# Performance work log

Hardware: AMD Instinct MI355X
Metric: run time of the kernel (lower is better)

The kernel has to match this reference:

```python
import jax, jax.numpy as jnp
import numpy as np

L, H, P = 8192, 512, 512


def setup_inputs() -> dict:
    key = jax.random.key(0)
    ks = jax.random.split(key, 7)
    u = jax.random.normal(ks[0], (L, H), dtype=jnp.float32)
    # diagonal continuous-time state matrix Lambda = Lambda_re + i*Lambda_im (stable: Re < 0)
    Lambda_re = -0.5 * jax.random.uniform(ks[1], (P,), dtype=jnp.float32) - 0.1
    Lambda_im = jnp.pi * jax.random.normal(ks[2], (P,), dtype=jnp.float32)
    # B_tilde (P,H) and C_tilde (H,P) parameterized as real/imag pairs (..., 2)
    B = jax.random.normal(ks[3], (P, H, 2), dtype=jnp.float32) / np.sqrt(2.0 * H)
    C = jax.random.normal(ks[4], (H, P, 2), dtype=jnp.float32) / np.sqrt(2.0 * P)
    D = jax.random.normal(ks[5], (H,), dtype=jnp.float32)
    log_step = jax.random.uniform(ks[6], (P,), dtype=jnp.float32,
                                  minval=np.log(1e-3), maxval=np.log(1e-1))
    return {"u": u, "Lambda_re": Lambda_re, "Lambda_im": Lambda_im,
            "B": B, "C": C, "D": D, "log_step": log_step}


def _binop(qi, qj):
    # binary operator for parallel scan of diagonal linear recurrence
    A_i, Bu_i = qi
    A_j, Bu_j = qj
    return (A_j * A_i, A_j * Bu_i + Bu_j)


def reference(u, Lambda_re, Lambda_im, B, C, D, log_step):
    Lambda = (Lambda_re + 1j * Lambda_im).astype(jnp.complex64)          # (P,)
    B_tilde = (B[..., 0] + 1j * B[..., 1]).astype(jnp.complex64)         # (P,H)
    C_tilde = (C[..., 0] + 1j * C[..., 1]).astype(jnp.complex64)         # (H,P)
    Delta = jnp.exp(log_step)                                            # (P,)
    # zero-order-hold discretization
    Lambda_bar = jnp.exp(Lambda * Delta)                                 # (P,)
    B_bar = ((Lambda_bar - 1.0) / Lambda)[:, None] * B_tilde             # (P,H)
    # Bu_t = B_bar @ u_t for all t  -> (L,P)
    Bu = jnp.einsum('lh,ph->lp', u.astype(jnp.complex64), B_bar)
    A_elems = jnp.broadcast_to(Lambda_bar, (u.shape[0], P))              # (L,P)
    _, xs = jax.lax.associative_scan(_binop, (A_elems, Bu), axis=0)      # (L,P) states
    # y_t = Re(C_tilde @ x_t) + D * u_t
    y = jnp.einsum('lp,hp->lh', xs, C_tilde).real + D * u
    return y
```

## Files before the change

kernel.cpp:

```cpp
#include <hip/hip_runtime.h>
#include <hip/hip_bf16.h>

#define L_DIM 8192
#define H_DIM 512
#define P_DIM 512
#define CHUNK 32
#define NCHUNK (L_DIM / CHUNK)

typedef __attribute__((ext_vector_type(8))) short bf16x8;
typedef __attribute__((ext_vector_type(4))) float f32x4;

__device__ inline short f2bf(float x) {
    union { float f; unsigned u; } v; v.f = x;
    unsigned r = v.u + 0x7fffu + ((v.u >> 16) & 1u);
    return (short)(r >> 16);
}
__device__ inline float bflo2f(unsigned w) {
    union { unsigned u; float f; } v; v.u = w << 16; return v.f;
}
__device__ inline float bfhi2f(unsigned w) {
    union { unsigned u; float f; } v; v.u = w & 0xffff0000u; return v.f;
}

__device__ inline void gload_lds16(const void* g, void* l) {
    __builtin_amdgcn_global_load_lds(
        (const __attribute__((address_space(1))) unsigned int*)g,
        (__attribute__((address_space(3))) unsigned int*)l, 16, 0, 0);
}

__global__ __launch_bounds__(256) void k_prep(
        const float* __restrict__ Lre, const float* __restrict__ Lim,
        const float* __restrict__ Bin, const float* __restrict__ log_step,
        const float* __restrict__ Cin, const float* __restrict__ u,
        short* __restrict__ Bcat, short* __restrict__ Ccat,
        short* __restrict__ u_bf,
        float* __restrict__ lambda_bar, float* __restrict__ lambda_powN) {
    const int blk = blockIdx.x;
    const int tid = threadIdx.x;
    if (blk < P_DIM) {
        int p = blk;
        float lr = Lre[p], li = Lim[p];
        float dt = expf(log_step[p]);
        float ar = lr * dt, ai = li * dt;
        float er = expf(ar);
        float lbr = er * cosf(ai);
        float lbi = er * sinf(ai);
        float nr = lbr - 1.0f, ni = lbi;
        float den = lr * lr + li * li;
        float fr = (nr * lr + ni * li) / den;
        float fi = (ni * lr - nr * li) / den;
        if (tid == 0) {
            lambda_bar[2 * p] = lbr;
            lambda_bar[2 * p + 1] = lbi;
            float eN = expf(ar * (float)CHUNK);
            lambda_powN[2 * p] = eN * cosf(ai * (float)CHUNK);
            lambda_powN[2 * p + 1] = eN * sinf(ai * (float)CHUNK);
        }
        for (int h = tid; h < H_DIM; h += 256) {
            float br = Bin[((size_t)p * H_DIM + h) * 2 + 0];
            float bi = Bin[((size_t)p * H_DIM + h) * 2 + 1];
            Bcat[(size_t)(2 * p) * H_DIM + h] = f2bf(fr * br - fi * bi);
            Bcat[(size_t)(2 * p + 1) * H_DIM + h] = f2bf(fr * bi + fi * br);
        }
    } else if (blk < P_DIM + 1024) {
        int idx = (blk - P_DIM) * 256 + tid;
        int h = idx >> 9, p = idx & 511;
        float cr = Cin[(size_t)idx * 2 + 0];
        float ci = Cin[(size_t)idx * 2 + 1];
        Ccat[(size_t)h * (2 * P_DIM) + 2 * p + 0] = f2bf(cr);
        Ccat[(size_t)h * (2 * P_DIM) + 2 * p + 1] = f2bf(-ci);
    } else {
        int i = (blk - P_DIM - 1024) * 256 + tid;
        const float4* uf = (const float4*)u;
        float4 a0 = uf[(size_t)i * 2];
        float4 a1 = uf[(size_t)i * 2 + 1];
        bf16x8 sv;
        sv[0] = f2bf(a0.x); sv[1] = f2bf(a0.y); sv[2] = f2bf(a0.z); sv[3] = f2bf(a0.w);
        sv[4] = f2bf(a1.x); sv[5] = f2bf(a1.y); sv[6] = f2bf(a1.z); sv[7] = f2bf(a1.w);
        *(bf16x8*)&u_bf[(size_t)i * 8] = sv;
    }
}

template<bool OBF16, bool EPI>
__global__ __launch_bounds__(256) void k_gemm(
        const short* __restrict__ A, const short* __restrict__ B,
        void* __restrict__ Cout, int M, int N, int K, int nwgn,
        const float* __restrict__ Dv, const short* __restrict__ Ubf) {
    __shared__ short As[2][128 * 32];
    __shared__ short Bs[2][128 * 32];
    const int tid = threadIdx.x;
    const int lane = tid & 63;
    const int wid = tid >> 6;
    const int wr = wid >> 1, wc = wid & 1;

    const int nwg = gridDim.x;
    const int orig = blockIdx.x;
    const int id = (orig & 7) * (nwg >> 3) + (orig >> 3);
    const int bm = (id / nwgn) * 128;
    const int bn = (id % nwgn) * 128;

    const int sbyte = wid * 2048 + lane * 16;
    const int srow = sbyte >> 6;
    const int scol = sbyte & 63;

    f32x4 acc[4][4] = {};
    const int arow = wr * 64 + (lane & 15);
    const int brow = wc * 64 + (lane & 15);
    const int kgrp = (lane >> 4) * 8;

    auto stage = [&](int buf, int kk) {
        const char* a0 = (const char*)A + ((size_t)(bm + srow) * K + kk) * 2 + scol;
        gload_lds16(a0, (char*)&As[buf][0] + sbyte);
        const char* a1 = (const char*)A + ((size_t)(bm + srow + 16) * K + kk) * 2 + scol;
        gload_lds16(a1, (char*)&As[buf][0] + sbyte + 1024);
        const char* b0 = (const char*)B + ((size_t)(bn + srow) * K + kk) * 2 + scol;
        gload_lds16(b0, (char*)&Bs[buf][0] + sbyte);
        const char* b1 = (const char*)B + ((size_t)(bn + srow + 16) * K + kk) * 2 + scol;
        gload_lds16(b1, (char*)&Bs[buf][0] + sbyte + 1024);
    };

    stage(0, 0);
    __syncthreads();

    int cur = 0;
    const int nt = K >> 5;
    for (int t = 0; t < nt; ++t) {
        if (t + 1 < nt) stage(cur ^ 1, (t + 1) * 32);
        bf16x8 af[4], bfr[4];
#pragma unroll
        for (int m = 0; m < 4; ++m) af[m] = *(const bf16x8*)&As[cur][(arow + m * 16) * 32 + kgrp];
#pragma unroll
        for (int n = 0; n < 4; ++n) bfr[n] = *(const bf16x8*)&Bs[cur][(brow + n * 16) * 32 + kgrp];
#pragma unroll
        for (int m = 0; m < 4; ++m)
#pragma unroll
            for (int n = 0; n < 4; ++n)
                acc[m][n] = __builtin_amdgcn_mfma_f32_16x16x32_bf16(af[m], bfr[n], acc[m][n], 0, 0, 0);
        __syncthreads();
        cur ^= 1;
    }

    const int fq = lane >> 4, fr = lane & 15;
#pragma unroll
    for (int m = 0; m < 4; ++m) {
#pragma unroll
        for (int n = 0; n < 4; ++n) {
            int col = bn + wc * 64 + n * 16 + fr;
            int row0 = bm + wr * 64 + m * 16 + fq * 4;
#pragma unroll
            for (int j = 0; j < 4; ++j) {
                int row = row0 + j;
                float v = acc[m][n][j];
                if (OBF16) {
                    ((short*)Cout)[(size_t)row * N + col] = f2bf(v);
                } else {
                    if (EPI) {
                        union { unsigned u; float f; } ub;
                        ub.u = ((unsigned)(unsigned short)Ubf[(size_t)row * N + col]) << 16;
                        v += Dv[col] * ub.f;
                    }
                    ((float*)Cout)[(size_t)row * N + col] = v;
                }
            }
        }
    }
}

__global__ __launch_bounds__(256) void k_scan_summary(const unsigned* __restrict__ Bu,
                                                      const float* __restrict__ lambda_bar,
                                                      float* __restrict__ S) {
    int gid = blockIdx.x * blockDim.x + threadIdx.x;
    int c = gid >> 9, p = gid & 511;
    float lr = lambda_bar[2 * p], li = lambda_bar[2 * p + 1];
    float xr = 0.f, xi = 0.f;
    const unsigned* bu = Bu + (size_t)c * CHUNK * P_DIM + p;
#pragma unroll 4
    for (int j = 0; j < CHUNK; ++j) {
        unsigned w = bu[(size_t)j * P_DIM];
        float br = bflo2f(w), bi = bfhi2f(w);
        float nxr = lr * xr - li * xi + br;
        float nxi = lr * xi + li * xr + bi;
        xr = nxr; xi = nxi;
    }
    ((float2*)S)[(size_t)c * P_DIM + p] = make_float2(xr, xi);
}

__global__ __launch_bounds__(512) void k_scan_apply(const unsigned* __restrict__ Bu,
                                                    unsigned* __restrict__ XsB,
                                                    const float* __restrict__ lambda_bar,
                                                    const float* __restrict__ lambda_powN,
                                                    const float* __restrict__ S) {
    const int c = blockIdx.x;
    const int p = threadIdx.x;
    const float lNr = lambda_powN[2 * p], lNi = lambda_powN[2 * p + 1];
    float xr = 0.f, xi = 0.f;
    const float2* Sp = (const float2*)S;
    int d = 0;
    while (d + 8 <= c) {
        float2 sb[8];
#pragma unroll
        for (int j = 0; j < 8; ++j) sb[j] = Sp[(size_t)(d + j) * P_DIM + p];
#pragma unroll
        for (int j = 0; j < 8; ++j) {
            float nxr = lNr * xr - lNi * xi + sb[j].x;
            float nxi = lNr * xi + lNi * xr + sb[j].y;
            xr = nxr; xi = nxi;
        }
        d += 8;
    }
    for (; d < c; ++d) {
        float2 s = Sp[(size_t)d * P_DIM + p];
        float nxr = lNr * xr - lNi * xi + s.x;
        float nxi = lNr * xi + lNi * xr + s.y;
        xr = nxr; xi = nxi;
    }
    const float lr = lambda_bar[2 * p], li = lambda_bar[2 * p + 1];
    const unsigned* bu = Bu + (size_t)c * CHUNK * P_DIM + p;
#pragma unroll 4
    for (int j = 0; j < CHUNK; ++j) {
        unsigned w = bu[(size_t)j * P_DIM];
        float br = bflo2f(w), bi = bfhi2f(w);
        float nxr = lr * xr - li * xi + br;
        float nxi = lr * xi + li * xr + bi;
        xr = nxr; xi = nxi;
        unsigned pk = (unsigned)(unsigned short)f2bf(xr)
                    | ((unsigned)(unsigned short)f2bf(xi) << 16);
        XsB[((size_t)c * CHUNK + j) * P_DIM + p] = pk;
    }
}

extern "C" void kernel_launch(void* const* d_in, const int* in_sizes, int n_in,
                              void* d_out, int out_size, void* d_ws, size_t ws_size,
                              hipStream_t stream) {
    const float* u        = (const float*)d_in[0];
    const float* Lre      = (const float*)d_in[1];
    const float* Lim      = (const float*)d_in[2];
    const float* Bin      = (const float*)d_in[3];
    const float* Cin      = (const float*)d_in[4];
    const float* Dv       = (const float*)d_in[5];
    const float* log_step = (const float*)d_in[6];
    float* y = (float*)d_out;

    char* w = (char*)d_ws;
    size_t off = 0;
    short* Bcat = (short*)(w + off); off += (size_t)2 * P_DIM * H_DIM * 2;
    short* Ccat = (short*)(w + off); off += (size_t)2 * P_DIM * H_DIM * 2;
    float* lamb = (float*)(w + off); off += 2 * P_DIM * 4;
    float* lamN = (float*)(w + off); off += 2 * P_DIM * 4;
    float* S    = (float*)(w + off); off += (size_t)NCHUNK * 2 * P_DIM * 4;
    unsigned* Bu  = (unsigned*)(w + off); off += (size_t)L_DIM * P_DIM * 4;
    unsigned* XsB = (unsigned*)(w + off); off += (size_t)L_DIM * P_DIM * 4;
    short* u_bf   = (short*)(w + off);   off += (size_t)L_DIM * H_DIM * 2;

    k_prep<<<P_DIM + 1024 + 2048, 256, 0, stream>>>(
        Lre, Lim, Bin, log_step, Cin, u, Bcat, Ccat, u_bf, lamb, lamN);
    k_gemm<true, false><<<(L_DIM / 128) * ((2 * P_DIM) / 128), 256, 0, stream>>>(
        u_bf, Bcat, (void*)Bu, L_DIM, 2 * P_DIM, H_DIM, (2 * P_DIM) / 128,
        nullptr, nullptr);
    k_scan_summary<<<(NCHUNK * P_DIM) / 256, 256, 0, stream>>>(Bu, lamb, S);
    k_scan_apply<<<NCHUNK, 512, 0, stream>>>(Bu, XsB, lamb, lamN, S);
    k_gemm<false, true><<<(L_DIM / 128) * (H_DIM / 128), 256, 0, stream>>>(
        (const short*)XsB, Ccat, (void*)y, L_DIM, H_DIM, 2 * P_DIM, H_DIM / 128,
        Dv, u_bf);
}
```

Measured before the change: 81.61 us.

## Triple-buffer GEMM LDS staging with XOR swizzle and narrower tiles for second GEMM

Rewrites the bf16 MFMA GEMM main loop to use three LDS buffers with two tiles in flight, replacing __syncthreads with explicit vmcnt waits and raw barriers. LDS reads and writes get an XOR swizzle to cut bank conflicts on the fragment loads. The output GEMM switches to 128x64 tiles, doubling its workgroup count to fill more CUs. The cost is extra LDS use and hand-written wait counts that must match the number of loads issued per stage.

```diff
diff --git a/kernel.cpp b/kernel.cpp
--- a/kernel.cpp
+++ b/kernel.cpp
@@ -26,6 +26,14 @@
     __builtin_amdgcn_global_load_lds(
         (const __attribute__((address_space(1))) unsigned int*)g,
         (__attribute__((address_space(3))) unsigned int*)l, 16, 0, 0);
+}
+
+template<int N> __device__ inline void waitcnt_vm() {
+    if constexpr (N == 0)      asm volatile("s_waitcnt vmcnt(0)" ::: "memory");
+    else if constexpr (N == 3) asm volatile("s_waitcnt vmcnt(3)" ::: "memory");
+    else if constexpr (N == 4) asm volatile("s_waitcnt vmcnt(4)" ::: "memory");
+    else if constexpr (N == 6) asm volatile("s_waitcnt vmcnt(6)" ::: "memory");
+    else if constexpr (N == 8) asm volatile("s_waitcnt vmcnt(8)" ::: "memory");
 }
 
 __global__ __launch_bounds__(256) void k_prep(
@@ -81,13 +89,16 @@
     }
 }
 
-template<bool OBF16, bool EPI>
+template<int BN, bool OBF16, bool EPI>
 __global__ __launch_bounds__(256) void k_gemm(
         const short* __restrict__ A, const short* __restrict__ B,
         void* __restrict__ Cout, int M, int N, int K, int nwgn,
         const float* __restrict__ Dv, const short* __restrict__ Ubf) {
-    __shared__ short As[2][128 * 32];
-    __shared__ short Bs[2][128 * 32];
+    constexpr int NF = BN / 32;
+    constexpr int LPS = 2 + BN / 64;
+    __shared__ short As[3][128 * 32];
+    __shared__ short Bs[3][BN * 32];
+
     const int tid = threadIdx.x;
     const int lane = tid & 63;
     const int wid = tid >> 6;
@@ -97,55 +108,75 @@
     const int orig = blockIdx.x;
     const int id = (orig & 7) * (nwg >> 3) + (orig >> 3);
     const int bm = (id / nwgn) * 128;
-    const int bn = (id % nwgn) * 128;
-
-    const int sbyte = wid * 2048 + lane * 16;
-    const int srow = sbyte >> 6;
-    const int scol = sbyte & 63;
-
-    f32x4 acc[4][4] = {};
+    const int bn = (id % nwgn) * BN;
+
+    f32x4 acc[4][NF] = {};
     const int arow = wr * 64 + (lane & 15);
-    const int brow = wc * 64 + (lane & 15);
-    const int kgrp = (lane >> 4) * 8;
+    const int brow = wc * (BN / 2) + (lane & 15);
+    const int rslot = (((lane >> 4) ^ (lane & 3) ^ ((lane >> 2) & 3)) << 4);
 
     auto stage = [&](int buf, int kk) {
-        const char* a0 = (const char*)A + ((size_t)(bm + srow) * K + kk) * 2 + scol;
-        gload_lds16(a0, (char*)&As[buf][0] + sbyte);
-        const char* a1 = (const char*)A + ((size_t)(bm + srow + 16) * K + kk) * 2 + scol;
-        gload_lds16(a1, (char*)&As[buf][0] + sbyte + 1024);
-        const char* b0 = (const char*)B + ((size_t)(bn + srow) * K + kk) * 2 + scol;
-        gload_lds16(b0, (char*)&Bs[buf][0] + sbyte);
-        const char* b1 = (const char*)B + ((size_t)(bn + srow + 16) * K + kk) * 2 + scol;
-        gload_lds16(b1, (char*)&Bs[buf][0] + sbyte + 1024);
+#pragma unroll
+        for (int q = 0; q < 2; ++q) {
+            int sb = q * 4096 + tid * 16;
+            int row = sb >> 6, slot = (sb >> 4) & 3;
+            int gs = slot ^ ((row ^ (row >> 2)) & 3);
+            const char* src = (const char*)A + ((size_t)(bm + row) * K + kk) * 2 + gs * 16;
+            gload_lds16(src, (char*)&As[buf][0] + sb);
+        }
+#pragma unroll
+        for (int q = 0; q < BN / 64; ++q) {
+            int sb = q * 4096 + tid * 16;
+            int row = sb >> 6, slot = (sb >> 4) & 3;
+            int gs = slot ^ ((row ^ (row >> 2)) & 3);
+            const char* src = (const char*)B + ((size_t)(bn + row) * K + kk) * 2 + gs * 16;
+            gload_lds16(src, (char*)&Bs[buf][0] + sb);
+        }
     };
 
+    const int nt = K >> 5;
     stage(0, 0);
-    __syncthreads();
-
-    int cur = 0;
-    const int nt = K >> 5;
+    stage(1, 32);
+
+    int cur = 0, stg = 2;
     for (int t = 0; t < nt; ++t) {
-        if (t + 1 < nt) stage(cur ^ 1, (t + 1) * 32);
-        bf16x8 af[4], bfr[4];
-#pragma unroll
-        for (int m = 0; m < 4; ++m) af[m] = *(const bf16x8*)&As[cur][(arow + m * 16) * 32 + kgrp];
-#pragma unroll
-        for (int n = 0; n < 4; ++n) bfr[n] = *(const bf16x8*)&Bs[cur][(brow + n * 16) * 32 + kgrp];
+        if (t + 2 < nt) {
+            stage(stg, (t + 2) * 32);
+            waitcnt_vm<2 * LPS>();
+        } else if (t + 1 < nt) {
+            waitcnt_vm<LPS>();
+        } else {
+            waitcnt_vm<0>();
+        }
+        __builtin_amdgcn_s_barrier();
+        __builtin_amdgcn_sched_barrier(0);
+
+        const char* Ab = (const char*)&As[cur][0];
+        const char* Bb = (const char*)&Bs[cur][0];
+        bf16x8 af[4], bfr[NF];
 #pragma unroll
         for (int m = 0; m < 4; ++m)
-#pragma unroll
-            for (int n = 0; n < 4; ++n)
+            af[m] = *(const bf16x8*)(Ab + (arow + m * 16) * 64 + rslot);
+#pragma unroll
+        for (int n = 0; n < NF; ++n)
+            bfr[n] = *(const bf16x8*)(Bb + (brow + n * 16) * 64 + rslot);
+#pragma unroll
+        for (int m = 0; m < 4; ++m)
+#pragma unroll
+            for (int n = 0; n < NF; ++n)
                 acc[m][n] = __builtin_amdgcn_mfma_f32_16x16x32_bf16(af[m], bfr[n], acc[m][n], 0, 0, 0);
-        __syncthreads();
-        cur ^= 1;
+
+        if (t + 1 < nt) __builtin_amdgcn_s_barrier();
+        cur = (cur == 2) ? 0 : cur + 1;
+        stg = (stg == 2) ? 0 : stg + 1;
     }
 
     const int fq = lane >> 4, fr = lane & 15;
 #pragma unroll
     for (int m = 0; m < 4; ++m) {
 #pragma unroll
-        for (int n = 0; n < 4; ++n) {
-            int col = bn + wc * 64 + n * 16 + fr;
+        for (int n = 0; n < NF; ++n) {
+            int col = bn + wc * (BN / 2) + n * 16 + fr;
             int row0 = bm + wr * 64 + m * 16 + fq * 4;
 #pragma unroll
             for (int j = 0; j < 4; ++j) {
@@ -254,12 +285,12 @@
 
     k_prep<<<P_DIM + 1024 + 2048, 256, 0, stream>>>(
         Lre, Lim, Bin, log_step, Cin, u, Bcat, Ccat, u_bf, lamb, lamN);
-    k_gemm<true, false><<<(L_DIM / 128) * ((2 * P_DIM) / 128), 256, 0, stream>>>(
+    k_gemm<128, true, false><<<(L_DIM / 128) * ((2 * P_DIM) / 128), 256, 0, stream>>>(
         u_bf, Bcat, (void*)Bu, L_DIM, 2 * P_DIM, H_DIM, (2 * P_DIM) / 128,
         nullptr, nullptr);
     k_scan_summary<<<(NCHUNK * P_DIM) / 256, 256, 0, stream>>>(Bu, lamb, S);
     k_scan_apply<<<NCHUNK, 512, 0, stream>>>(Bu, XsB, lamb, lamN, S);
-    k_gemm<false, true><<<(L_DIM / 128) * (H_DIM / 128), 256, 0, stream>>>(
-        (const short*)XsB, Ccat, (void*)y, L_DIM, H_DIM, 2 * P_DIM, H_DIM / 128,
+    k_gemm<64, false, true><<<(L_DIM / 128) * (H_DIM / 64), 256, 0, stream>>>(
+        (const short*)XsB, Ccat, (void*)y, L_DIM, H_DIM, 2 * P_DIM, H_DIM / 64,
         Dv, u_bf);
 }
```

After: 78.91 us. -3.3%, faster.
